# Kernel tuning notes

Hardware: AMD Instinct MI355X
Metric: run time of the kernel (lower is better)

## Reference

```python
import jax, jax.numpy as jnp
import numpy as np

N = 100_000  # nodes
E = 1_600_000  # edges (before self-loops)
NEG_SLOPE = 0.2  # PyG GATConv default leaky_relu slope


def gat_layer(x, W, a_src, a_dst, b, src, dst, heads, out_ch, concat):
    # x: [N, Fin]; W: [Fin, heads*out_ch]; a_src/a_dst: [1, heads, out_ch]
    h = (x @ W).reshape(-1, heads, out_ch)            # [N, H, C]
    alpha_s = jnp.sum(h * a_src, axis=-1)             # [N, H]
    alpha_d = jnp.sum(h * a_dst, axis=-1)             # [N, H]
    e = jax.nn.leaky_relu(alpha_s[src] + alpha_d[dst], NEG_SLOPE)  # [E', H]
    # softmax over edges grouped by destination node (self-loops guarantee
    # every node has at least one incoming edge)
    m = jax.ops.segment_max(e, dst, num_segments=N)   # [N, H]
    p = jnp.exp(e - m[dst])                           # [E', H]
    s = jax.ops.segment_sum(p, dst, num_segments=N)   # [N, H]
    alpha = p / s[dst]                                # [E', H]
    out = jax.ops.segment_sum(alpha[:, :, None] * h[src], dst, num_segments=N)  # [N,H,C]
    out = out.reshape(-1, heads * out_ch) if concat else out.mean(axis=1)
    return out + b


def setup_inputs() -> dict:
    key = jax.random.key(0)
    ks = jax.random.split(key, 8)

    def glorot(k, shape):
        return (jax.random.normal(k, shape, jnp.float32) / np.sqrt(np.float32(shape[0]))).astype(jnp.float32)

    x = jax.random.normal(ks[0], (N, 512), jnp.float32)
    edge_index = jax.random.randint(ks[1], (2, E), 0, N, dtype=jnp.int64)
    W1 = glorot(ks[2], (512, 64))
    att_src1 = jax.random.normal(ks[3], (1, 8, 8), jnp.float32) * 0.1
    att_dst1 = jax.random.normal(ks[4], (1, 8, 8), jnp.float32) * 0.1
    b1 = jnp.zeros((64,), jnp.float32)
    W2 = glorot(ks[5], (64, 128))
    att_src2 = jax.random.normal(ks[6], (1, 1, 128), jnp.float32) * 0.1
    att_dst2 = jax.random.normal(ks[7], (1, 1, 128), jnp.float32) * 0.1
    b2 = jnp.zeros((128,), jnp.float32)
    return {"x": x, "edge_index": edge_index, "W1": W1, "att_src1": att_src1,
            "att_dst1": att_dst1, "b1": b1, "W2": W2, "att_src2": att_src2,
            "att_dst2": att_dst2, "b2": b2}


def reference(x, edge_index, W1, att_src1, att_dst1, b1, W2, att_src2, att_dst2, b2):
    # PyG GATConv adds self-loops by default
    loop = jnp.arange(N, dtype=edge_index.dtype)
    src = jnp.concatenate([edge_index[0], loop])
    dst = jnp.concatenate([edge_index[1], loop])
    h = gat_layer(x, W1, att_src1, att_dst1, b1, src, dst, heads=8, out_ch=8, concat=True)
    h = jax.nn.elu(h)
    z = gat_layer(h, W2, att_src2, att_dst2, b2, src, dst, heads=1, out_ch=128, concat=False)
    return z
```

## Files before the change

### kernel.cpp

```cpp
#include <hip/hip_runtime.h>
#include <math.h>

#define NNODES 100000

__device__ __forceinline__ float lrelu(float v) { return v > 0.f ? v : 0.2f * v; }

__global__ __launch_bounds__(256) void gemm1_k(const float* __restrict__ x,
                                               const float* __restrict__ W,
                                               float* __restrict__ h1, int Nn) {
    __shared__ float xs[64][65];
    __shared__ float ws[64][65];
    int r0 = blockIdx.x * 64;
    int t = threadIdx.x;
    int ty = t >> 4, tx = t & 15;
    float acc[4][4] = {};
    for (int kb = 0; kb < 512; kb += 64) {
        for (int l = t; l < 1024; l += 256) {
            int row = l >> 4;
            int c4 = (l & 15) * 4;
            int gr = r0 + row;
            float4 v = make_float4(0.f, 0.f, 0.f, 0.f);
            if (gr < Nn) v = *reinterpret_cast<const float4*>(&x[(size_t)gr * 512 + kb + c4]);
            xs[row][c4] = v.x; xs[row][c4 + 1] = v.y; xs[row][c4 + 2] = v.z; xs[row][c4 + 3] = v.w;
        }
        for (int l = t; l < 1024; l += 256) {
            int row = l >> 4;
            int c4 = (l & 15) * 4;
            float4 v = *reinterpret_cast<const float4*>(&W[(size_t)(kb + row) * 64 + c4]);
            ws[row][c4] = v.x; ws[row][c4 + 1] = v.y; ws[row][c4 + 2] = v.z; ws[row][c4 + 3] = v.w;
        }
        __syncthreads();
#pragma unroll 8
        for (int k = 0; k < 64; ++k) {
            float a[4], b[4];
#pragma unroll
            for (int i = 0; i < 4; ++i) a[i] = xs[ty * 4 + i][k];
#pragma unroll
            for (int j = 0; j < 4; ++j) b[j] = ws[k][tx * 4 + j];
#pragma unroll
            for (int i = 0; i < 4; ++i)
#pragma unroll
                for (int j = 0; j < 4; ++j) acc[i][j] += a[i] * b[j];
        }
        __syncthreads();
    }
#pragma unroll
    for (int i = 0; i < 4; ++i) {
        int gr = r0 + ty * 4 + i;
        if (gr < Nn) {
#pragma unroll
            for (int j = 0; j < 4; ++j) h1[(size_t)gr * 64 + tx * 4 + j] = acc[i][j];
        }
    }
}

__global__ __launch_bounds__(256) void gemm2_k(const float* __restrict__ xin,
                                               const float* __restrict__ W,
                                               float* __restrict__ h2, int Nn) {
    __shared__ float xs[64][65];
    __shared__ float ws[64][129];
    int r0 = blockIdx.x * 64;
    int t = threadIdx.x;
    int ty = t >> 4, tx = t & 15;
    for (int l = t; l < 1024; l += 256) {
        int row = l >> 4;
        int c4 = (l & 15) * 4;
        int gr = r0 + row;
        float4 v = make_float4(0.f, 0.f, 0.f, 0.f);
        if (gr < Nn) v = *reinterpret_cast<const float4*>(&xin[(size_t)gr * 64 + c4]);
        xs[row][c4] = v.x; xs[row][c4 + 1] = v.y; xs[row][c4 + 2] = v.z; xs[row][c4 + 3] = v.w;
    }
    for (int l = t; l < 2048; l += 256) {
        int row = l >> 5;
        int c4 = (l & 31) * 4;
        float4 v = *reinterpret_cast<const float4*>(&W[(size_t)row * 128 + c4]);
        ws[row][c4] = v.x; ws[row][c4 + 1] = v.y; ws[row][c4 + 2] = v.z; ws[row][c4 + 3] = v.w;
    }
    __syncthreads();
    float acc0[4][4] = {};
    float acc1[4][4] = {};
#pragma unroll 8
    for (int k = 0; k < 64; ++k) {
        float a[4], b0[4], b1[4];
#pragma unroll
        for (int i = 0; i < 4; ++i) a[i] = xs[ty * 4 + i][k];
#pragma unroll
        for (int j = 0; j < 4; ++j) { b0[j] = ws[k][tx * 4 + j]; b1[j] = ws[k][64 + tx * 4 + j]; }
#pragma unroll
        for (int i = 0; i < 4; ++i)
#pragma unroll
            for (int j = 0; j < 4; ++j) {
                acc0[i][j] += a[i] * b0[j];
                acc1[i][j] += a[i] * b1[j];
            }
    }
#pragma unroll
    for (int i = 0; i < 4; ++i) {
        int gr = r0 + ty * 4 + i;
        if (gr < Nn) {
#pragma unroll
            for (int j = 0; j < 4; ++j) {
                h2[(size_t)gr * 128 + tx * 4 + j] = acc0[i][j];
                h2[(size_t)gr * 128 + 64 + tx * 4 + j] = acc1[i][j];
            }
        }
    }
}

__global__ __launch_bounds__(256) void attn1_k(const float* __restrict__ h1,
                                               const float* __restrict__ asrc,
                                               const float* __restrict__ adst,
                                               float* __restrict__ as1,
                                               float* __restrict__ ad1, int Nn) {
    int t = blockIdx.x * 256 + threadIdx.x;
    int n = t >> 3, h = t & 7;
    if (n >= Nn) return;
    const float* hp = h1 + (size_t)n * 64 + h * 8;
    float s = 0.f, d = 0.f;
#pragma unroll
    for (int c = 0; c < 8; ++c) {
        float v = hp[c];
        s += v * asrc[h * 8 + c];
        d += v * adst[h * 8 + c];
    }
    as1[(size_t)n * 8 + h] = s;
    ad1[(size_t)n * 8 + h] = d;
}

__global__ __launch_bounds__(256) void attn2_k(const float* __restrict__ h2,
                                               const float* __restrict__ asrc,
                                               const float* __restrict__ adst,
                                               float* __restrict__ as2,
                                               float* __restrict__ ad2, int Nn) {
    int wid = threadIdx.x >> 6, lane = threadIdx.x & 63;
    int n = blockIdx.x * 4 + wid;
    if (n >= Nn) return;
    float v0 = h2[(size_t)n * 128 + lane];
    float v1 = h2[(size_t)n * 128 + 64 + lane];
    float s = v0 * asrc[lane] + v1 * asrc[64 + lane];
    float d = v0 * adst[lane] + v1 * adst[64 + lane];
#pragma unroll
    for (int off = 32; off >= 1; off >>= 1) {
        s += __shfl_xor(s, off);
        d += __shfl_xor(d, off);
    }
    if (lane == 0) { as2[n] = s; ad2[n] = d; }
}

__global__ __launch_bounds__(256) void hist_k(const int* __restrict__ ei, int E, int Etot,
                                              int* __restrict__ indeg) {
    int e = blockIdx.x * 256 + threadIdx.x;
    if (e >= Etot) return;
    int d = (e < E) ? ei[E + e] : (e - E);
    atomicAdd(&indeg[d], 1);
}

__global__ __launch_bounds__(256) void scanA_k(const int* __restrict__ indeg,
                                               int* __restrict__ indptr,
                                               int* __restrict__ bsums, int Nn) {
    __shared__ int sd[256];
    int t = threadIdx.x;
    int i0 = blockIdx.x * 2048 + t * 8;
    int v[8], ex[8];
    int run = 0;
#pragma unroll
    for (int j = 0; j < 8; ++j) {
        int i = i0 + j;
        v[j] = (i < Nn) ? indeg[i] : 0;
        ex[j] = run;
        run += v[j];
    }
    sd[t] = run;
    __syncthreads();
    for (int off = 1; off < 256; off <<= 1) {
        int a = (t >= off) ? sd[t - off] : 0;
        __syncthreads();
        sd[t] += a;
        __syncthreads();
    }
    int texc = sd[t] - run;
#pragma unroll
    for (int j = 0; j < 8; ++j) {
        int i = i0 + j;
        if (i < Nn) indptr[i] = texc + ex[j];
    }
    if (t == 0) bsums[blockIdx.x] = sd[255];
}

__global__ void scanB_k(int* __restrict__ bsums, int nb) {
    if (threadIdx.x == 0 && blockIdx.x == 0) {
        int run = 0;
        for (int b = 0; b < nb; ++b) {
            int x = bsums[b];
            bsums[b] = run;
            run += x;
        }
    }
}

__global__ __launch_bounds__(256) void scanC_k(int* __restrict__ indptr,
                                               const int* __restrict__ bsums,
                                               int* __restrict__ cursor, int Nn, int Etot) {
    int t = threadIdx.x;
    int b = blockIdx.x;
    int base = bsums[b];
    int i0 = b * 2048 + t * 8;
#pragma unroll
    for (int j = 0; j < 8; ++j) {
        int i = i0 + j;
        if (i < Nn) {
            int val = indptr[i] + base;
            indptr[i] = val;
            cursor[i] = val;
        }
    }
    if (b == 0 && t == 0) indptr[Nn] = Etot;
}

__global__ __launch_bounds__(256) void fill_k(const int* __restrict__ ei, int E, int Etot,
                                              int* __restrict__ cursor, int* __restrict__ col) {
    int e = blockIdx.x * 256 + threadIdx.x;
    if (e >= Etot) return;
    int s, d;
    if (e < E) { s = ei[e]; d = ei[E + e]; }
    else { s = e - E; d = e - E; }
    int pos = atomicAdd(&cursor[d], 1);
    col[pos] = s;
}

__global__ __launch_bounds__(256) void agg1_k(const float* __restrict__ h1,
                                              const float* __restrict__ as1,
                                              const float* __restrict__ ad1,
                                              const int* __restrict__ indptr,
                                              const int* __restrict__ col,
                                              const float* __restrict__ b1,
                                              float* __restrict__ h1a, int Nn) {
    int wid = threadIdx.x >> 6, lane = threadIdx.x & 63;
    int n = blockIdx.x * 4 + wid;
    if (n >= Nn) return;
    int beg = indptr[n], end = indptr[n + 1];
    int h = lane & 7, eo = lane >> 3;
    float adn = ad1[(size_t)n * 8 + h];
    float ss = 0.f;
    for (int i = beg + eo; i < end; i += 8) {
        int s = col[i];
        ss += __expf(lrelu(as1[(size_t)s * 8 + h] + adn));
    }
    ss += __shfl_xor(ss, 8);
    ss += __shfl_xor(ss, 16);
    ss += __shfl_xor(ss, 32);
    int hb = lane >> 3;
    float sb = __shfl(ss, hb);
    float ab = __shfl(adn, hb);
    float inv = 1.f / sb;
    const float* __restrict__ h1l = h1 + lane;
    float acc0 = 0.f, acc1 = 0.f, acc2 = 0.f, acc3 = 0.f;
    int i = beg;
    for (; i + 4 <= end; i += 4) {
        int s0 = col[i], s1 = col[i + 1], s2 = col[i + 2], s3 = col[i + 3];
        float w0 = __expf(lrelu(as1[(size_t)s0 * 8 + hb] + ab));
        float w1 = __expf(lrelu(as1[(size_t)s1 * 8 + hb] + ab));
        float w2 = __expf(lrelu(as1[(size_t)s2 * 8 + hb] + ab));
        float w3 = __expf(lrelu(as1[(size_t)s3 * 8 + hb] + ab));
        acc0 += w0 * h1l[(size_t)s0 * 64];
        acc1 += w1 * h1l[(size_t)s1 * 64];
        acc2 += w2 * h1l[(size_t)s2 * 64];
        acc3 += w3 * h1l[(size_t)s3 * 64];
    }
    for (; i < end; ++i) {
        int s = col[i];
        acc0 += __expf(lrelu(as1[(size_t)s * 8 + hb] + ab)) * h1l[(size_t)s * 64];
    }
    float o = ((acc0 + acc1) + (acc2 + acc3)) * inv + b1[lane];
    h1a[(size_t)n * 64 + lane] = o > 0.f ? o : expm1f(o);
}

__global__ __launch_bounds__(256) void agg2_k(const float* __restrict__ h2,
                                              const float* __restrict__ as2,
                                              const float* __restrict__ ad2,
                                              const int* __restrict__ indptr,
                                              const int* __restrict__ col,
                                              const float* __restrict__ b2,
                                              float* __restrict__ out, int Nn) {
    int wid = threadIdx.x >> 6, lane = threadIdx.x & 63;
    int n = blockIdx.x * 4 + wid;
    if (n >= Nn) return;
    int beg = indptr[n], end = indptr[n + 1];
    float adn = ad2[n];
    float ss = 0.f;
    for (int i = beg + lane; i < end; i += 64) {
        ss += __expf(lrelu(as2[col[i]] + adn));
    }
#pragma unroll
    for (int off = 32; off >= 1; off >>= 1) ss += __shfl_xor(ss, off);
    float inv = 1.f / ss;
    const float* __restrict__ h2l = h2 + lane;
    float a00 = 0.f, a01 = 0.f, a02 = 0.f, a03 = 0.f;
    float a10 = 0.f, a11 = 0.f, a12 = 0.f, a13 = 0.f;
    int i = beg;
    for (; i + 4 <= end; i += 4) {
        int s0 = col[i], s1 = col[i + 1], s2 = col[i + 2], s3 = col[i + 3];
        float w0 = __expf(lrelu(as2[s0] + adn));
        float w1 = __expf(lrelu(as2[s1] + adn));
        float w2 = __expf(lrelu(as2[s2] + adn));
        float w3 = __expf(lrelu(as2[s3] + adn));
        a00 += w0 * h2l[(size_t)s0 * 128];
        a10 += w0 * h2l[(size_t)s0 * 128 + 64];
        a01 += w1 * h2l[(size_t)s1 * 128];
        a11 += w1 * h2l[(size_t)s1 * 128 + 64];
        a02 += w2 * h2l[(size_t)s2 * 128];
        a12 += w2 * h2l[(size_t)s2 * 128 + 64];
        a03 += w3 * h2l[(size_t)s3 * 128];
        a13 += w3 * h2l[(size_t)s3 * 128 + 64];
    }
    for (; i < end; ++i) {
        int s = col[i];
        float w = __expf(lrelu(as2[s] + adn));
        a00 += w * h2l[(size_t)s * 128];
        a10 += w * h2l[(size_t)s * 128 + 64];
    }
    out[(size_t)n * 128 + lane] = ((a00 + a01) + (a02 + a03)) * inv + b2[lane];
    out[(size_t)n * 128 + 64 + lane] = ((a10 + a11) + (a12 + a13)) * inv + b2[64 + lane];
}

extern "C" void kernel_launch(void* const* d_in, const int* in_sizes, int n_in,
                              void* d_out, int out_size, void* d_ws, size_t ws_size,
                              hipStream_t stream) {
    const float* x = (const float*)d_in[0];
    const int* ei = (const int*)d_in[1];
    const float* W1 = (const float*)d_in[2];
    const float* asrc1 = (const float*)d_in[3];
    const float* adst1 = (const float*)d_in[4];
    const float* b1 = (const float*)d_in[5];
    const float* W2 = (const float*)d_in[6];
    const float* asrc2 = (const float*)d_in[7];
    const float* adst2 = (const float*)d_in[8];
    const float* b2 = (const float*)d_in[9];
    float* out = (float*)d_out;

    const int Nn = NNODES;
    const int E = in_sizes[1] / 2;
    const int Etot = E + Nn;

    char* w = (char*)d_ws;
    auto alloc = [&](size_t bytes) {
        char* p = w;
        w += (bytes + 255) & ~(size_t)255;
        return p;
    };
    float* h1 = (float*)alloc((size_t)Nn * 64 * 4);
    float* h1a = (float*)alloc((size_t)Nn * 64 * 4);
    float* h2 = (float*)alloc((size_t)Nn * 128 * 4);
    float* as1 = (float*)alloc((size_t)Nn * 8 * 4);
    float* ad1 = (float*)alloc((size_t)Nn * 8 * 4);
    float* as2 = (float*)alloc((size_t)Nn * 4);
    float* ad2 = (float*)alloc((size_t)Nn * 4);
    int* indeg = (int*)alloc((size_t)(Nn + 1) * 4);
    int* indptr = (int*)alloc((size_t)(Nn + 1) * 4);
    int* cursor = (int*)alloc((size_t)Nn * 4);
    int* bsums = (int*)alloc(4096);
    int* col = (int*)alloc((size_t)Etot * 4);

    const int NBLK = (Nn + 2047) / 2048;

    hipMemsetAsync(indeg, 0, (size_t)Nn * 4, stream);
    gemm1_k<<<(Nn + 63) / 64, 256, 0, stream>>>(x, W1, h1, Nn);
    attn1_k<<<(Nn * 8 + 255) / 256, 256, 0, stream>>>(h1, asrc1, adst1, as1, ad1, Nn);
    hist_k<<<(Etot + 255) / 256, 256, 0, stream>>>(ei, E, Etot, indeg);
    scanA_k<<<NBLK, 256, 0, stream>>>(indeg, indptr, bsums, Nn);
    scanB_k<<<1, 64, 0, stream>>>(bsums, NBLK);
    scanC_k<<<NBLK, 256, 0, stream>>>(indptr, bsums, cursor, Nn, Etot);
    fill_k<<<(Etot + 255) / 256, 256, 0, stream>>>(ei, E, Etot, cursor, col);
    agg1_k<<<(Nn + 3) / 4, 256, 0, stream>>>(h1, as1, ad1, indptr, col, b1, h1a, Nn);
    gemm2_k<<<(Nn + 63) / 64, 256, 0, stream>>>(h1a, W2, h2, Nn);
    attn2_k<<<(Nn + 3) / 4, 256, 0, stream>>>(h2, asrc2, adst2, as2, ad2, Nn);
    agg2_k<<<(Nn + 3) / 4, 256, 0, stream>>>(h2, as2, ad2, indptr, col, b2, out, Nn);
}
```

Before: 902.1 us.

## Transpose GEMM shared tiles, vectorize LDS/global access, enlarge gemm1 row tile

Both dense projection kernels now store the activation tile transposed in shared memory. This lets inner-loop operands be read as float4 vectors instead of scalar strided loads. Weight tiles are copied to LDS as float4, and outputs are written with float4 stores. gemm1 also handles 128 rows per block with 8x4 accumulators per thread, which halves the grid and raises reuse of the weight tile, at the cost of more registers and shared memory plus bank conflicts in the transposed scalar stores.

```diff
diff --git a/kernel.cpp b/kernel.cpp
--- a/kernel.cpp
+++ b/kernel.cpp
@@ -8,48 +8,48 @@
 __global__ __launch_bounds__(256) void gemm1_k(const float* __restrict__ x,
                                                const float* __restrict__ W,
                                                float* __restrict__ h1, int Nn) {
-    __shared__ float xs[64][65];
-    __shared__ float ws[64][65];
-    int r0 = blockIdx.x * 64;
+    __shared__ float xs[64][132];
+    __shared__ float ws[64][68];
+    int r0 = blockIdx.x * 128;
     int t = threadIdx.x;
     int ty = t >> 4, tx = t & 15;
-    float acc[4][4] = {};
+    float acc[8][4] = {};
     for (int kb = 0; kb < 512; kb += 64) {
-        for (int l = t; l < 1024; l += 256) {
+        for (int l = t; l < 2048; l += 256) {
             int row = l >> 4;
             int c4 = (l & 15) * 4;
             int gr = r0 + row;
             float4 v = make_float4(0.f, 0.f, 0.f, 0.f);
             if (gr < Nn) v = *reinterpret_cast<const float4*>(&x[(size_t)gr * 512 + kb + c4]);
-            xs[row][c4] = v.x; xs[row][c4 + 1] = v.y; xs[row][c4 + 2] = v.z; xs[row][c4 + 3] = v.w;
+            xs[c4][row] = v.x; xs[c4 + 1][row] = v.y; xs[c4 + 2][row] = v.z; xs[c4 + 3][row] = v.w;
         }
         for (int l = t; l < 1024; l += 256) {
             int row = l >> 4;
             int c4 = (l & 15) * 4;
-            float4 v = *reinterpret_cast<const float4*>(&W[(size_t)(kb + row) * 64 + c4]);
-            ws[row][c4] = v.x; ws[row][c4 + 1] = v.y; ws[row][c4 + 2] = v.z; ws[row][c4 + 3] = v.w;
+            *reinterpret_cast<float4*>(&ws[row][c4]) =
+                *reinterpret_cast<const float4*>(&W[(size_t)(kb + row) * 64 + c4]);
         }
         __syncthreads();
-#pragma unroll 8
+#pragma unroll 4
         for (int k = 0; k < 64; ++k) {
-            float a[4], b[4];
-#pragma unroll
-            for (int i = 0; i < 4; ++i) a[i] = xs[ty * 4 + i][k];
-#pragma unroll
-            for (int j = 0; j < 4; ++j) b[j] = ws[k][tx * 4 + j];
-#pragma unroll
-            for (int i = 0; i < 4; ++i)
+            float4 a0 = *reinterpret_cast<const float4*>(&xs[k][ty * 8]);
+            float4 a1 = *reinterpret_cast<const float4*>(&xs[k][ty * 8 + 4]);
+            float4 bv = *reinterpret_cast<const float4*>(&ws[k][tx * 4]);
+            float a[8] = {a0.x, a0.y, a0.z, a0.w, a1.x, a1.y, a1.z, a1.w};
+            float b[4] = {bv.x, bv.y, bv.z, bv.w};
+#pragma unroll
+            for (int i = 0; i < 8; ++i)
 #pragma unroll
                 for (int j = 0; j < 4; ++j) acc[i][j] += a[i] * b[j];
         }
         __syncthreads();
     }
 #pragma unroll
-    for (int i = 0; i < 4; ++i) {
-        int gr = r0 + ty * 4 + i;
+    for (int i = 0; i < 8; ++i) {
+        int gr = r0 + ty * 8 + i;
         if (gr < Nn) {
-#pragma unroll
-            for (int j = 0; j < 4; ++j) h1[(size_t)gr * 64 + tx * 4 + j] = acc[i][j];
+            float4 o = make_float4(acc[i][0], acc[i][1], acc[i][2], acc[i][3]);
+            *reinterpret_cast<float4*>(&h1[(size_t)gr * 64 + tx * 4]) = o;
         }
     }
 }
@@ -57,8 +57,8 @@
 __global__ __launch_bounds__(256) void gemm2_k(const float* __restrict__ xin,
                                                const float* __restrict__ W,
                                                float* __restrict__ h2, int Nn) {
-    __shared__ float xs[64][65];
-    __shared__ float ws[64][129];
+    __shared__ float xs[64][68];
+    __shared__ float ws[64][132];
     int r0 = blockIdx.x * 64;
     int t = threadIdx.x;
     int ty = t >> 4, tx = t & 15;
@@ -68,24 +68,25 @@
         int gr = r0 + row;
         float4 v = make_float4(0.f, 0.f, 0.f, 0.f);
         if (gr < Nn) v = *reinterpret_cast<const float4*>(&xin[(size_t)gr * 64 + c4]);
-        xs[row][c4] = v.x; xs[row][c4 + 1] = v.y; xs[row][c4 + 2] = v.z; xs[row][c4 + 3] = v.w;
+        xs[c4][row] = v.x; xs[c4 + 1][row] = v.y; xs[c4 + 2][row] = v.z; xs[c4 + 3][row] = v.w;
     }
     for (int l = t; l < 2048; l += 256) {
         int row = l >> 5;
         int c4 = (l & 31) * 4;
-        float4 v = *reinterpret_cast<const float4*>(&W[(size_t)row * 128 + c4]);
-        ws[row][c4] = v.x; ws[row][c4 + 1] = v.y; ws[row][c4 + 2] = v.z; ws[row][c4 + 3] = v.w;
+        *reinterpret_cast<float4*>(&ws[row][c4]) =
+            *reinterpret_cast<const float4*>(&W[(size_t)row * 128 + c4]);
     }
     __syncthreads();
     float acc0[4][4] = {};
     float acc1[4][4] = {};
-#pragma unroll 8
+#pragma unroll 4
     for (int k = 0; k < 64; ++k) {
-        float a[4], b0[4], b1[4];
-#pragma unroll
-        for (int i = 0; i < 4; ++i) a[i] = xs[ty * 4 + i][k];
-#pragma unroll
-        for (int j = 0; j < 4; ++j) { b0[j] = ws[k][tx * 4 + j]; b1[j] = ws[k][64 + tx * 4 + j]; }
+        float4 av = *reinterpret_cast<const float4*>(&xs[k][ty * 4]);
+        float4 b0v = *reinterpret_cast<const float4*>(&ws[k][tx * 4]);
+        float4 b1v = *reinterpret_cast<const float4*>(&ws[k][64 + tx * 4]);
+        float a[4] = {av.x, av.y, av.z, av.w};
+        float b0[4] = {b0v.x, b0v.y, b0v.z, b0v.w};
+        float b1[4] = {b1v.x, b1v.y, b1v.z, b1v.w};
 #pragma unroll
         for (int i = 0; i < 4; ++i)
 #pragma unroll
@@ -98,11 +99,10 @@
     for (int i = 0; i < 4; ++i) {
         int gr = r0 + ty * 4 + i;
         if (gr < Nn) {
-#pragma unroll
-            for (int j = 0; j < 4; ++j) {
-                h2[(size_t)gr * 128 + tx * 4 + j] = acc0[i][j];
-                h2[(size_t)gr * 128 + 64 + tx * 4 + j] = acc1[i][j];
-            }
+            float4 o0 = make_float4(acc0[i][0], acc0[i][1], acc0[i][2], acc0[i][3]);
+            float4 o1 = make_float4(acc1[i][0], acc1[i][1], acc1[i][2], acc1[i][3]);
+            *reinterpret_cast<float4*>(&h2[(size_t)gr * 128 + tx * 4]) = o0;
+            *reinterpret_cast<float4*>(&h2[(size_t)gr * 128 + 64 + tx * 4]) = o1;
         }
     }
 }
@@ -364,7 +364,7 @@
     const int NBLK = (Nn + 2047) / 2048;
 
     hipMemsetAsync(indeg, 0, (size_t)Nn * 4, stream);
-    gemm1_k<<<(Nn + 63) / 64, 256, 0, stream>>>(x, W1, h1, Nn);
+    gemm1_k<<<(Nn + 127) / 128, 256, 0, stream>>>(x, W1, h1, Nn);
     attn1_k<<<(Nn * 8 + 255) / 256, 256, 0, stream>>>(h1, asrc1, adst1, as1, ad1, Nn);
     hist_k<<<(Etot + 255) / 256, 256, 0, stream>>>(ei, E, Etot, indeg);
     scanA_k<<<NBLK, 256, 0, stream>>>(indeg, indptr, bsums, Nn);
```

New measurement: 877.9 us. 2.7% less time.
